# Kernel optimization log

Hardware: AMD Instinct MI355X
Metric: run time of the kernel (lower is better)

Reference implementation:

```python
import jax, jax.numpy as jnp
import numpy as np


def _apply_rope(t, cos, sin):
    # t: [b, s, h, d]; cos/sin: [s, d//2]; interleaved complex rotation
    b, s, h, d = t.shape
    tr = t.reshape(b, s, h, d // 2, 2)
    a, bb = tr[..., 0], tr[..., 1]
    c = cos[None, :, None, :]
    si = sin[None, :, None, :]
    out_r = a * c - bb * si
    out_i = a * si + bb * c
    return jnp.stack([out_r, out_i], axis=-1).reshape(b, s, h, d)


def setup_inputs() -> dict:
    key = jax.random.key(0)
    ks = jax.random.split(key, 10)
    B, S, D = 4, 512, 4096
    H, HKV, HD = 32, 8, 128
    START = 512
    wscale = 0.02  # keep activations in sane range
    x = jax.random.normal(ks[0], (B, S, D), dtype=jnp.float32)
    wq = jax.random.normal(ks[1], (H * HD, D), dtype=jnp.float32) * wscale
    wk = jax.random.normal(ks[2], (HKV * HD, D), dtype=jnp.float32) * wscale
    wv = jax.random.normal(ks[3], (HKV * HD, D), dtype=jnp.float32) * wscale
    wo = jax.random.normal(ks[4], (D, H * HD), dtype=jnp.float32) * wscale
    # RoPE angles for absolute positions [START, START+S)
    theta = 500000.0
    inv_freq = 1.0 / (theta ** (np.arange(0, HD, 2, dtype=np.float32) / HD))
    pos = np.arange(START, START + S, dtype=np.float32)
    ang = pos[:, None] * inv_freq[None, :]  # [S, HD//2]
    freqs_cos = jnp.asarray(np.cos(ang), dtype=jnp.float32)
    freqs_sin = jnp.asarray(np.sin(ang), dtype=jnp.float32)
    cache_k = jax.random.normal(ks[5], (B, START, HKV, HD), dtype=jnp.float32)
    cache_v = jax.random.normal(ks[6], (B, START, HKV, HD), dtype=jnp.float32)
    return {"x": x, "wq": wq, "wk": wk, "wv": wv, "wo": wo,
            "freqs_cos": freqs_cos, "freqs_sin": freqs_sin,
            "cache_k": cache_k, "cache_v": cache_v, "start_pos": START}


def reference(x, wq, wk, wv, wo, freqs_cos, freqs_sin, cache_k, cache_v, start_pos):
    B, S, D = x.shape
    H = wq.shape[0] // 128
    HKV = wk.shape[0] // 128
    HD = 128
    n_rep = H // HKV
    # QKV projections (Linear: y = x @ W^T)
    xq = jnp.einsum('bsd,ed->bse', x, wq).reshape(B, S, H, HD)
    xk = jnp.einsum('bsd,ed->bse', x, wk).reshape(B, S, HKV, HD)
    xv = jnp.einsum('bsd,ed->bse', x, wv).reshape(B, S, HKV, HD)
    # rotary embedding on new q/k
    xq = _apply_rope(xq, freqs_cos, freqs_sin)
    xk = _apply_rope(xk, freqs_cos, freqs_sin)
    # append new k/v to cache -> total kv length T = start_pos + S
    keys = jnp.concatenate([cache_k, xk], axis=1)    # [B, T, HKV, HD]
    values = jnp.concatenate([cache_v, xv], axis=1)  # [B, T, HKV, HD]
    # GQA: repeat kv heads (repeat_interleave along head dim)
    keys = jnp.repeat(keys, n_rep, axis=2)      # [B, T, H, HD]
    values = jnp.repeat(values, n_rep, axis=2)  # [B, T, H, HD]
    scores = jnp.einsum('bqhd,bkhd->bhqk', xq, keys) / jnp.sqrt(jnp.float32(HD))
    # causal mask: query abs pos start_pos+i attends to kv pos <= start_pos+i
    T = start_pos + S
    q_pos = start_pos + jnp.arange(S)
    k_pos = jnp.arange(T)
    mask = k_pos[None, :] <= q_pos[:, None]  # [S, T]
    scores = jnp.where(mask[None, None, :, :], scores, -jnp.inf)
    probs = jax.nn.softmax(scores.astype(jnp.float32), axis=-1).astype(x.dtype)
    out = jnp.einsum('bhqk,bkhd->bqhd', probs, values).reshape(B, S, H * HD)
    return jnp.einsum('bse,de->bsd', out, wo)
```

## Files before the change

### kernel.cpp

```cpp
#include <hip/hip_runtime.h>
#include <hip/hip_bf16.h>


#define B_ 4
#define S_ 512
#define D_ 4096
#define H_ 32
#define HKV_ 8
#define HD_ 128
#define T_ 1024
#define M_ 2048
#define NQKV_ 6144

typedef __attribute__((ext_vector_type(8))) short bf16x8;
typedef __attribute__((ext_vector_type(4))) float f32x4;

#define GLOAD_LDS16(g, l)                                                     \
  __builtin_amdgcn_global_load_lds(                                           \
      (const __attribute__((address_space(1))) void*)(g),                     \
      (__attribute__((address_space(3))) void*)(l), 16, 0, 0)

__device__ __forceinline__ void st_c(float* p, float v) { *p = v; }
__device__ __forceinline__ void st_c(__hip_bfloat16* p, float v) {
  *p = __float2bfloat16(v);
}

__global__ void cvt_f32_bf16(const float* __restrict__ in,
                             __hip_bfloat16* __restrict__ out, long n) {
  long i = ((long)blockIdx.x * blockDim.x + threadIdx.x) * 4;
  if (i >= n) return;
  float4 v = *(const float4*)(in + i);
  __hip_bfloat16 t[4] = {__float2bfloat16(v.x), __float2bfloat16(v.y),
                         __float2bfloat16(v.z), __float2bfloat16(v.w)};
  *(uint2*)(out + i) = *(const uint2*)t;
}

template <typename CT>
__global__ __launch_bounds__(256) void gemm_nt(
    const __hip_bfloat16* __restrict__ A, const __hip_bfloat16* __restrict__ B,
    CT* __restrict__ C, int M, int N, int K, long ldA, long ldB, long ldC,
    int Hdiv, int rep, long sAb, long sAh, long sBb, long sBh, long sCb,
    long sCh) {
  int z = blockIdx.z;
  int zb = z / Hdiv, zh = z - zb * Hdiv;
  A += (long)zb * sAb + (long)zh * sAh;
  B += (long)zb * sBb + (long)(zh / rep) * sBh;
  C += (long)zb * sCb + (long)zh * sCh;

  const int m0 = blockIdx.y * 128;
  const int n0 = blockIdx.x * 128;
  const int tid = threadIdx.x;
  const int wave = tid >> 6, lane = tid & 63;
  const int wm = (wave >> 1) * 64, wn = (wave & 1) * 64;

  __shared__ __align__(16) __hip_bfloat16 As[128 * 32];
  __shared__ __align__(16) __hip_bfloat16 Bs[128 * 32];

  const int slot0 = tid, slot1 = 256 + tid;
  const int r0 = slot0 >> 2, c0 = (slot0 & 3) ^ ((r0 >> 1) & 3);
  const int r1 = slot1 >> 2, c1 = (slot1 & 3) ^ ((r1 >> 1) & 3);
  const __hip_bfloat16* gA0 = A + (long)(m0 + r0) * ldA + c0 * 8;
  const __hip_bfloat16* gA1 = A + (long)(m0 + r1) * ldA + c1 * 8;
  const __hip_bfloat16* gB0 = B + (long)(n0 + r0) * ldB + c0 * 8;
  const __hip_bfloat16* gB1 = B + (long)(n0 + r1) * ldB + c1 * 8;
  __hip_bfloat16* sA0 = &As[wave * 512];
  __hip_bfloat16* sA1 = &As[2048 + wave * 512];
  __hip_bfloat16* sB0 = &Bs[wave * 512];
  __hip_bfloat16* sB1 = &Bs[2048 + wave * 512];

  const int lr = lane & 15;
  const int sfrag = (lane >> 4) ^ ((lr >> 1) & 3);
  const int abase = (wm + lr) * 32 + sfrag * 8;
  const int bbase = (wn + lr) * 32 + sfrag * 8;

  f32x4 acc[4][4];
#pragma unroll
  for (int i = 0; i < 4; i++)
#pragma unroll
    for (int j = 0; j < 4; j++) acc[i][j] = f32x4{0.f, 0.f, 0.f, 0.f};

  for (int kt = 0; kt < K; kt += 32) {
    GLOAD_LDS16(gA0, sA0);
    GLOAD_LDS16(gA1, sA1);
    GLOAD_LDS16(gB0, sB0);
    GLOAD_LDS16(gB1, sB1);
    gA0 += 32;
    gA1 += 32;
    gB0 += 32;
    gB1 += 32;
    __syncthreads();

    bf16x8 af[4], bfv[4];
#pragma unroll
    for (int i = 0; i < 4; i++) {
      af[i] = *(const bf16x8*)&As[abase + i * 512];
      bfv[i] = *(const bf16x8*)&Bs[bbase + i * 512];
    }
#pragma unroll
    for (int i = 0; i < 4; i++)
#pragma unroll
      for (int j = 0; j < 4; j++)
        acc[i][j] =
            __builtin_amdgcn_mfma_f32_16x16x32_bf16(af[i], bfv[j], acc[i][j],
                                                    0, 0, 0);
    __syncthreads();
  }

  const int crow0 = m0 + wm + (lane >> 4) * 4;
  const int ccol0 = n0 + wn + (lane & 15);
#pragma unroll
  for (int i = 0; i < 4; i++)
#pragma unroll
    for (int j = 0; j < 4; j++)
#pragma unroll
      for (int r = 0; r < 4; r++)
        st_c(&C[(long)(crow0 + i * 16 + r) * ldC + (ccol0 + j * 16)],
             acc[i][j][r]);
}

__global__ __launch_bounds__(256, 2) void flash_attn(
    const __hip_bfloat16* __restrict__ qb,
    const __hip_bfloat16* __restrict__ kb,
    const __hip_bfloat16* __restrict__ vtb,
    __hip_bfloat16* __restrict__ ob) {
  const int qt = 3 - blockIdx.x;
  const int z = blockIdx.y;
  const int b = z >> 5, h = z & 31, kvh = h >> 2;
  const int q0 = qt * 128;
  const int tid = threadIdx.x, wave = tid >> 6, lane = tid & 63;
  const int lr = lane & 15, lq = lane >> 4;
  const int wrow = wave * 32;
  const float scale = 0.08838834764831845f;

  __shared__ __align__(16) __hip_bfloat16 smem[64 * 128 + 128 * 64 + 128 * 72];
  __hip_bfloat16* Ks = smem;
  __hip_bfloat16* Vs = smem + 64 * 128;
  __hip_bfloat16* Ps = smem + 64 * 128 + 128 * 64;
  __hip_bfloat16* Os = smem;

  const __hip_bfloat16* Kz = kb + ((long)(b * 8 + kvh)) * T_ * HD_;
  const __hip_bfloat16* Vz = vtb + ((long)(b * 8 + kvh)) * HD_ * T_;
  const __hip_bfloat16* Qz = qb + ((long)(b * 512 + q0)) * 4096 + h * 128;
  __hip_bfloat16* obz = ob + ((long)(b * 512 + q0)) * 4096 + h * 128;

  bf16x8 qf[2][4];
#pragma unroll
  for (int i = 0; i < 2; i++)
#pragma unroll
    for (int kb4 = 0; kb4 < 4; kb4++)
      qf[i][kb4] = *(const bf16x8*)(Qz + (long)(wrow + i * 16 + lr) * 4096 +
                                    kb4 * 32 + lq * 8);

  int kOff[4], vOff[4];
#pragma unroll
  for (int it = 0; it < 4; it++) {
    int G = it * 256 + tid;
    int t = G >> 4, ck = (G & 15) ^ (t & 7);
    kOff[it] = t * 128 + ck * 8;
    int d = G >> 3, cv = (G & 7) ^ (d & 7);
    vOff[it] = d * 1024 + cv * 8;
  }

  f32x4 O[2][8];
#pragma unroll
  for (int i = 0; i < 2; i++)
#pragma unroll
    for (int j = 0; j < 8; j++) O[i][j] = f32x4{0.f, 0.f, 0.f, 0.f};
  float mst[2][4], lst[2][4];
#pragma unroll
  for (int i = 0; i < 2; i++)
#pragma unroll
    for (int r = 0; r < 4; r++) {
      mst[i][r] = -1e30f;
      lst[i][r] = 0.f;
    }

  const int ntiles = 10 + 2 * qt, fulltiles = 8 + 2 * qt;
  const int hxor = lr & 7;

  for (int kt = 0; kt < ntiles; kt++) {
    const int k0 = kt * 64;
#pragma unroll
    for (int it = 0; it < 4; it++)
      GLOAD_LDS16(Kz + (long)k0 * 128 + kOff[it],
                  Ks + (it * 256 + wave * 64) * 8);
#pragma unroll
    for (int it = 0; it < 4; it++)
      GLOAD_LDS16(Vz + k0 + vOff[it], Vs + (it * 256 + wave * 64) * 8);
    __syncthreads();

    f32x4 s[2][4];
#pragma unroll
    for (int i = 0; i < 2; i++)
#pragma unroll
      for (int j = 0; j < 4; j++) s[i][j] = f32x4{0.f, 0.f, 0.f, 0.f};
#pragma unroll
    for (int kb4 = 0; kb4 < 4; kb4++) {
      bf16x8 kf[4];
#pragma unroll
      for (int j = 0; j < 4; j++)
        kf[j] = *(const bf16x8*)(Ks + (j * 16 + lr) * 128 +
                                 ((kb4 * 4 + lq) ^ hxor) * 8);
#pragma unroll
      for (int i = 0; i < 2; i++)
#pragma unroll
        for (int j = 0; j < 4; j++)
          s[i][j] = __builtin_amdgcn_mfma_f32_16x16x32_bf16(qf[i][kb4], kf[j],
                                                            s[i][j], 0, 0, 0);
    }

    const bool mt = (kt >= fulltiles);
#pragma unroll
    for (int i = 0; i < 2; i++)
#pragma unroll
      for (int j = 0; j < 4; j++)
#pragma unroll
        for (int r = 0; r < 4; r++) {
          float sv = s[i][j][r] * scale;
          if (mt) {
            int key = k0 + j * 16 + lr;
            int qp = 512 + q0 + wrow + i * 16 + lq * 4 + r;
            if (key > qp) sv = -1e30f;
          }
          s[i][j][r] = sv;
        }

    float al[2][4];
#pragma unroll
    for (int i = 0; i < 2; i++)
#pragma unroll
      for (int r = 0; r < 4; r++) {
        float mx = fmaxf(fmaxf(s[i][0][r], s[i][1][r]),
                         fmaxf(s[i][2][r], s[i][3][r]));
        mx = fmaxf(mx, __shfl_xor(mx, 1));
        mx = fmaxf(mx, __shfl_xor(mx, 2));
        mx = fmaxf(mx, __shfl_xor(mx, 4));
        mx = fmaxf(mx, __shfl_xor(mx, 8));
        float mn = fmaxf(mst[i][r], mx);
        al[i][r] = __expf(mst[i][r] - mn);
        mst[i][r] = mn;
      }
#pragma unroll
    for (int i = 0; i < 2; i++)
#pragma unroll
      for (int j = 0; j < 4; j++)
#pragma unroll
        for (int r = 0; r < 4; r++)
          s[i][j][r] = __expf(s[i][j][r] - mst[i][r]);
#pragma unroll
    for (int i = 0; i < 2; i++)
#pragma unroll
      for (int r = 0; r < 4; r++) {
        float sm = s[i][0][r] + s[i][1][r] + s[i][2][r] + s[i][3][r];
        sm += __shfl_xor(sm, 1);
        sm += __shfl_xor(sm, 2);
        sm += __shfl_xor(sm, 4);
        sm += __shfl_xor(sm, 8);
        lst[i][r] = lst[i][r] * al[i][r] + sm;
      }
#pragma unroll
    for (int i = 0; i < 2; i++)
#pragma unroll
      for (int j = 0; j < 8; j++)
#pragma unroll
        for (int r = 0; r < 4; r++) O[i][j][r] *= al[i][r];

#pragma unroll
    for (int i = 0; i < 2; i++)
#pragma unroll
      for (int j = 0; j < 4; j++)
#pragma unroll
        for (int r = 0; r < 4; r++)
          Ps[(wrow + i * 16 + lq * 4 + r) * 72 + j * 16 + lr] =
              __float2bfloat16(s[i][j][r]);

#pragma unroll
    for (int kc = 0; kc < 2; kc++) {
      bf16x8 pa[2];
#pragma unroll
      for (int i = 0; i < 2; i++)
        pa[i] = *(const bf16x8*)(Ps + (wrow + i * 16 + lr) * 72 + kc * 32 +
                                 lq * 8);
      bf16x8 vf[8];
#pragma unroll
      for (int j = 0; j < 8; j++)
        vf[j] = *(const bf16x8*)(Vs + (j * 16 + lr) * 64 +
                                 ((kc * 4 + lq) ^ hxor) * 8);
#pragma unroll
      for (int i = 0; i < 2; i++)
#pragma unroll
        for (int j = 0; j < 8; j++)
          O[i][j] = __builtin_amdgcn_mfma_f32_16x16x32_bf16(pa[i], vf[j],
                                                            O[i][j], 0, 0, 0);
    }
    __syncthreads();
  }

#pragma unroll
  for (int i = 0; i < 2; i++)
#pragma unroll
    for (int r = 0; r < 4; r++) {
      float inv = 1.f / lst[i][r];
#pragma unroll
      for (int j = 0; j < 8; j++)
        Os[(wrow + i * 16 + lq * 4 + r) * 136 + j * 16 + lr] =
            __float2bfloat16(O[i][j][r] * inv);
    }
  __syncthreads();
#pragma unroll
  for (int it = 0; it < 8; it++) {
    int G = it * 256 + tid;
    int m = G >> 4, c = G & 15;
    *(bf16x8*)(obz + (long)m * 4096 + c * 8) =
        *(const bf16x8*)(Os + m * 136 + c * 8);
  }
}

__global__ void rope_kernel(const float* __restrict__ qkv,
                            const float* __restrict__ fcos,
                            const float* __restrict__ fsin,
                            __hip_bfloat16* __restrict__ qb,
                            __hip_bfloat16* __restrict__ kb) {
  int m = blockIdx.y;
  int j = blockIdx.x * blockDim.x + threadIdx.x;
  if (j >= 2560) return;
  int s = m & (S_ - 1);
  long rowbase = (long)m * NQKV_;
  if (j < 2048) {
    int dpair = j & 63;
    float a = qkv[rowbase + 2 * j], bb = qkv[rowbase + 2 * j + 1];
    float c = fcos[s * 64 + dpair], si = fsin[s * 64 + dpair];
    long o = (long)m * 4096 + 2 * j;
    qb[o] = __float2bfloat16(a * c - bb * si);
    qb[o + 1] = __float2bfloat16(a * si + bb * c);
  } else {
    int j2 = j - 2048;
    int kvh = j2 >> 6, dpair = j2 & 63;
    float a = qkv[rowbase + 4096 + 2 * j2], bb = qkv[rowbase + 4096 + 2 * j2 + 1];
    float c = fcos[s * 64 + dpair], si = fsin[s * 64 + dpair];
    int b = m >> 9;
    long o = (((long)(b * HKV_ + kvh)) * T_ + 512 + s) * HD_ + 2 * dpair;
    kb[o] = __float2bfloat16(a * c - bb * si);
    kb[o + 1] = __float2bfloat16(a * si + bb * c);
  }
}

__global__ void kcache_cvt(const float* __restrict__ cache_k,
                           __hip_bfloat16* __restrict__ kb) {
  long i = (long)blockIdx.x * 256 + threadIdx.x;
  if (i >= (long)B_ * HKV_ * 512 * HD_) return;
  int d = i & 127;
  int t = (i >> 7) & 511;
  int kvh = (i >> 16) & 7;
  int b = i >> 19;
  long o = (((long)(b * HKV_ + kvh)) * T_ + t) * HD_ + d;
  kb[o] = __float2bfloat16(
      cache_k[(((long)(b * 512 + t)) * HKV_ + kvh) * HD_ + d]);
}

__global__ void v_transpose(const float* __restrict__ cache_v,
                            const float* __restrict__ qkv,
                            __hip_bfloat16* __restrict__ vtb) {
  __shared__ float tile[32][33];
  int t0 = blockIdx.x * 32, d0 = blockIdx.y * 32;
  int bk = blockIdx.z;
  int b = bk >> 3, kvh = bk & 7;
#pragma unroll
  for (int it = 0; it < 4; it++) {
    int t = t0 + threadIdx.y + it * 8;
    int d = d0 + threadIdx.x;
    float v;
    if (t < 512)
      v = cache_v[(((long)(b * 512 + t)) * HKV_ + kvh) * HD_ + d];
    else
      v = qkv[((long)(b * S_) + (t - 512)) * NQKV_ + 5120 + kvh * HD_ + d];
    tile[threadIdx.y + it * 8][threadIdx.x] = v;
  }
  __syncthreads();
#pragma unroll
  for (int it = 0; it < 4; it++) {
    int d = d0 + threadIdx.y + it * 8;
    int t = t0 + threadIdx.x;
    vtb[((long)bk * HD_ + d) * T_ + t] =
        __float2bfloat16(tile[threadIdx.x][threadIdx.y + it * 8]);
  }
}

extern "C" void kernel_launch(void* const* d_in, const int* in_sizes, int n_in,
                              void* d_out, int out_size, void* d_ws,
                              size_t ws_size, hipStream_t stream) {
  const float* x = (const float*)d_in[0];
  const float* wq = (const float*)d_in[1];
  const float* wk = (const float*)d_in[2];
  const float* wv = (const float*)d_in[3];
  const float* wo = (const float*)d_in[4];
  const float* fcos = (const float*)d_in[5];
  const float* fsin = (const float*)d_in[6];
  const float* cache_k = (const float*)d_in[7];
  const float* cache_v = (const float*)d_in[8];
  float* out = (float*)d_out;

  char* ws = (char*)d_ws;
  const size_t szR0 = (size_t)M_ * 4096 * 2;
  const size_t szR1 = (size_t)NQKV_ * D_ * 2;
  const size_t szR2 = (size_t)M_ * NQKV_ * 4;
  const size_t szKV = (size_t)B_ * HKV_ * T_ * HD_ * 2;

  size_t R0 = 0;
  size_t R1 = R0 + szR0;
  size_t R2 = R1 + szR1;
  size_t R3 = R2 + szR2;
  size_t R4 = R3 + szKV;

  __hip_bfloat16* xb = (__hip_bfloat16*)(ws + R0);
  __hip_bfloat16* wqkvb = (__hip_bfloat16*)(ws + R1);
  float* qkvf = (float*)(ws + R2);
  __hip_bfloat16* kb = (__hip_bfloat16*)(ws + R3);
  __hip_bfloat16* vtb = (__hip_bfloat16*)(ws + R4);

  dim3 blk(256);

  cvt_f32_bf16<<<(M_ * (long)D_ / 4 + 255) / 256, blk, 0, stream>>>(
      x, xb, (long)M_ * D_);
  cvt_f32_bf16<<<((long)D_ * D_ / 4 + 255) / 256, blk, 0, stream>>>(
      wq, wqkvb, (long)D_ * D_);
  cvt_f32_bf16<<<((long)1024 * D_ / 4 + 255) / 256, blk, 0, stream>>>(
      wk, wqkvb + (long)4096 * D_, (long)1024 * D_);
  cvt_f32_bf16<<<((long)1024 * D_ / 4 + 255) / 256, blk, 0, stream>>>(
      wv, wqkvb + (long)5120 * D_, (long)1024 * D_);

  gemm_nt<float><<<dim3(NQKV_ / 128, M_ / 128, 1), blk, 0, stream>>>(
      xb, wqkvb, qkvf, M_, NQKV_, D_, D_, D_, NQKV_, 1, 1, 0, 0, 0, 0, 0, 0);

  __hip_bfloat16* qb = xb;
  rope_kernel<<<dim3(10, M_), blk, 0, stream>>>(qkvf, fcos, fsin, qb, kb);

  kcache_cvt<<<((long)B_ * HKV_ * 512 * HD_ + 255) / 256, blk, 0, stream>>>(
      cache_k, kb);
  v_transpose<<<dim3(T_ / 32, HD_ / 32, B_ * HKV_), dim3(32, 8), 0, stream>>>(
      cache_v, qkvf, vtb);

  __hip_bfloat16* wob = wqkvb;
  cvt_f32_bf16<<<((long)D_ * D_ / 4 + 255) / 256, blk, 0, stream>>>(
      wo, wob, (long)D_ * D_);

  __hip_bfloat16* ob = xb;
  flash_attn<<<dim3(4, B_ * H_), blk, 0, stream>>>(qb, kb, vtb, ob);

  gemm_nt<float><<<dim3(D_ / 128, M_ / 128, 1), blk, 0, stream>>>(
      ob, wob, out, M_, D_, D_, D_, D_, D_, 1, 1, 0, 0, 0, 0, 0, 0);
}
```

Baseline: 560.6 us.

## Replace 128x128 GEMM with double-buffered 256x256 tile GEMM with XCD swizzle

The QKV and output projections now use a new GEMM with 256x256 tiles, 512 threads and a 64-wide K step. The K step is split into two 32-wide halves across a double-buffered LDS ring, so global-to-LDS loads for the next tile are issued while MFMAs on the current tile run. Barriers and s_setprio raise the priority of the MFMA phases. The workgroup index is remapped so neighbouring tiles land on the same XCD for L2 reuse. The aim is to cut the load/compute serialisation and global traffic of the old single-buffered kernel, at the cost of more LDS (128KB) and more registers per block.

```diff
diff --git a/kernel.cpp b/kernel.cpp
--- a/kernel.cpp
+++ b/kernel.cpp
@@ -20,11 +20,6 @@
       (const __attribute__((address_space(1))) void*)(g),                     \
       (__attribute__((address_space(3))) void*)(l), 16, 0, 0)
 
-__device__ __forceinline__ void st_c(float* p, float v) { *p = v; }
-__device__ __forceinline__ void st_c(__hip_bfloat16* p, float v) {
-  *p = __float2bfloat16(v);
-}
-
 __global__ void cvt_f32_bf16(const float* __restrict__ in,
                              __hip_bfloat16* __restrict__ out, long n) {
   long i = ((long)blockIdx.x * blockDim.x + threadIdx.x) * 4;
@@ -35,87 +30,154 @@
   *(uint2*)(out + i) = *(const uint2*)t;
 }
 
-template <typename CT>
-__global__ __launch_bounds__(256) void gemm_nt(
+__global__ __launch_bounds__(512, 2) void gemm256(
     const __hip_bfloat16* __restrict__ A, const __hip_bfloat16* __restrict__ B,
-    CT* __restrict__ C, int M, int N, int K, long ldA, long ldB, long ldC,
-    int Hdiv, int rep, long sAb, long sAh, long sBb, long sBh, long sCb,
-    long sCh) {
-  int z = blockIdx.z;
-  int zb = z / Hdiv, zh = z - zb * Hdiv;
-  A += (long)zb * sAb + (long)zh * sAh;
-  B += (long)zb * sBb + (long)(zh / rep) * sBh;
-  C += (long)zb * sCb + (long)zh * sCh;
-
-  const int m0 = blockIdx.y * 128;
-  const int n0 = blockIdx.x * 128;
+    float* __restrict__ C, int M, int N, int K, long ldA, long ldB, long ldC) {
+  const int nbx = N >> 8;
+  const int nwg = nbx * (M >> 8);
+  const int lin = blockIdx.x + nbx * blockIdx.y;
+  const int cpx = nwg >> 3;
+  const int swz = (lin & 7) * cpx + (lin >> 3);
+  const int m0 = (swz / nbx) << 8;
+  const int n0 = (swz - (swz / nbx) * nbx) << 8;
+
   const int tid = threadIdx.x;
-  const int wave = tid >> 6, lane = tid & 63;
-  const int wm = (wave >> 1) * 64, wn = (wave & 1) * 64;
-
-  __shared__ __align__(16) __hip_bfloat16 As[128 * 32];
-  __shared__ __align__(16) __hip_bfloat16 Bs[128 * 32];
-
-  const int slot0 = tid, slot1 = 256 + tid;
-  const int r0 = slot0 >> 2, c0 = (slot0 & 3) ^ ((r0 >> 1) & 3);
-  const int r1 = slot1 >> 2, c1 = (slot1 & 3) ^ ((r1 >> 1) & 3);
-  const __hip_bfloat16* gA0 = A + (long)(m0 + r0) * ldA + c0 * 8;
-  const __hip_bfloat16* gA1 = A + (long)(m0 + r1) * ldA + c1 * 8;
-  const __hip_bfloat16* gB0 = B + (long)(n0 + r0) * ldB + c0 * 8;
-  const __hip_bfloat16* gB1 = B + (long)(n0 + r1) * ldB + c1 * 8;
-  __hip_bfloat16* sA0 = &As[wave * 512];
-  __hip_bfloat16* sA1 = &As[2048 + wave * 512];
-  __hip_bfloat16* sB0 = &Bs[wave * 512];
-  __hip_bfloat16* sB1 = &Bs[2048 + wave * 512];
-
-  const int lr = lane & 15;
-  const int sfrag = (lane >> 4) ^ ((lr >> 1) & 3);
-  const int abase = (wm + lr) * 32 + sfrag * 8;
-  const int bbase = (wn + lr) * 32 + sfrag * 8;
-
-  f32x4 acc[4][4];
-#pragma unroll
-  for (int i = 0; i < 4; i++)
+  const int w = tid >> 6, l = tid & 63;
+  const int wm = w >> 2, wn = w & 3;
+  const int lr = l & 15, lq = l >> 4;
+
+  __shared__ __align__(16) __hip_bfloat16 smem[8][8192];
+
+  const int rS = w * 16 + (l >> 2);
+  const int cS = (l & 3) ^ ((rS >> 1) & 3);
+  const __hip_bfloat16* gA = A + (long)(m0 + rS) * ldA + cS * 8;
+  const __hip_bfloat16* gB = B + (long)(n0 + rS) * ldB + cS * 8;
+  const long stA = 128 * ldA, stB = 128 * ldB;
+  const int wofs = w * 512;
+
+  const int cR = (lq ^ ((lr >> 1) & 3)) * 8;
+  const int aOff = (wm * 128 + lr) * 32 + cR;
+  const int bOff = (wn * 64 + lr) * 32 + cR;
+
+  f32x4 acc[8][4];
+#pragma unroll
+  for (int i = 0; i < 8; i++)
 #pragma unroll
     for (int j = 0; j < 4; j++) acc[i][j] = f32x4{0.f, 0.f, 0.f, 0.f};
 
-  for (int kt = 0; kt < K; kt += 32) {
-    GLOAD_LDS16(gA0, sA0);
-    GLOAD_LDS16(gA1, sA1);
-    GLOAD_LDS16(gB0, sB0);
-    GLOAD_LDS16(gB1, sB1);
-    gA0 += 32;
-    gA1 += 32;
-    gB0 += 32;
-    gB1 += 32;
-    __syncthreads();
-
-    bf16x8 af[4], bfv[4];
-#pragma unroll
-    for (int i = 0; i < 4; i++) {
-      af[i] = *(const bf16x8*)&As[abase + i * 512];
-      bfv[i] = *(const bf16x8*)&Bs[bbase + i * 512];
-    }
+  const int nkt = K >> 6;
+
+#define STAGE_A(buf, kh, ko)                                  \
+  {                                                           \
+    const __hip_bfloat16* g_ = gA + (ko) + (kh) * 32;         \
+    __hip_bfloat16* d_ = &smem[(buf) * 4 + (kh)][wofs];       \
+    GLOAD_LDS16(g_, d_);                                      \
+    GLOAD_LDS16(g_ + stA, d_ + 4096);                         \
+  }
+#define STAGE_B(buf, kh, ko)                                  \
+  {                                                           \
+    const __hip_bfloat16* g_ = gB + (ko) + (kh) * 32;         \
+    __hip_bfloat16* d_ = &smem[(buf) * 4 + 2 + (kh)][wofs];   \
+    GLOAD_LDS16(g_, d_);                                      \
+    GLOAD_LDS16(g_ + stB, d_ + 4096);                         \
+  }
+
+  STAGE_A(0, 0, 0);
+  STAGE_B(0, 0, 0);
+  STAGE_A(0, 1, 0);
+  STAGE_B(0, 1, 0);
+  asm volatile("s_waitcnt vmcnt(4)" ::: "memory");
+  __builtin_amdgcn_s_barrier();
+
+  bf16x8 af[4], bfr[4];
+  for (int t = 0; t < nkt; ++t) {
+    const int b = t & 1;
+    int tn = t + 1;
+    if (tn == nkt) tn = 0;
+    const long ko = (long)tn << 6;
+    const __hip_bfloat16* rA0 = &smem[b * 4 + 0][0];
+    const __hip_bfloat16* rA1 = &smem[b * 4 + 1][0];
+    const __hip_bfloat16* rB0 = &smem[b * 4 + 2][0];
+    const __hip_bfloat16* rB1 = &smem[b * 4 + 3][0];
+
+#pragma unroll
+    for (int i = 0; i < 4; i++) af[i] = *(const bf16x8*)(rA0 + aOff + i * 512);
+#pragma unroll
+    for (int j = 0; j < 4; j++) bfr[j] = *(const bf16x8*)(rB0 + bOff + j * 512);
+    STAGE_A(b ^ 1, 0, ko);
+    __builtin_amdgcn_s_barrier();
+    __builtin_amdgcn_s_setprio(1);
 #pragma unroll
     for (int i = 0; i < 4; i++)
 #pragma unroll
       for (int j = 0; j < 4; j++)
-        acc[i][j] =
-            __builtin_amdgcn_mfma_f32_16x16x32_bf16(af[i], bfv[j], acc[i][j],
-                                                    0, 0, 0);
-    __syncthreads();
-  }
-
-  const int crow0 = m0 + wm + (lane >> 4) * 4;
-  const int ccol0 = n0 + wn + (lane & 15);
-#pragma unroll
-  for (int i = 0; i < 4; i++)
+        acc[i][j] = __builtin_amdgcn_mfma_f32_16x16x32_bf16(af[i], bfr[j],
+                                                            acc[i][j], 0, 0, 0);
+    __builtin_amdgcn_s_setprio(0);
+    __builtin_amdgcn_s_barrier();
+
+#pragma unroll
+    for (int i = 0; i < 4; i++)
+      af[i] = *(const bf16x8*)(rA0 + aOff + (i + 4) * 512);
+    STAGE_B(b ^ 1, 0, ko);
+    asm volatile("s_waitcnt vmcnt(4)" ::: "memory");
+    __builtin_amdgcn_s_barrier();
+    __builtin_amdgcn_s_setprio(1);
+#pragma unroll
+    for (int i = 0; i < 4; i++)
+#pragma unroll
+      for (int j = 0; j < 4; j++)
+        acc[i + 4][j] = __builtin_amdgcn_mfma_f32_16x16x32_bf16(
+            af[i], bfr[j], acc[i + 4][j], 0, 0, 0);
+    __builtin_amdgcn_s_setprio(0);
+    __builtin_amdgcn_s_barrier();
+
+#pragma unroll
+    for (int i = 0; i < 4; i++) af[i] = *(const bf16x8*)(rA1 + aOff + i * 512);
+#pragma unroll
+    for (int j = 0; j < 4; j++) bfr[j] = *(const bf16x8*)(rB1 + bOff + j * 512);
+    STAGE_A(b ^ 1, 1, ko);
+    __builtin_amdgcn_s_barrier();
+    __builtin_amdgcn_s_setprio(1);
+#pragma unroll
+    for (int i = 0; i < 4; i++)
+#pragma unroll
+      for (int j = 0; j < 4; j++)
+        acc[i][j] = __builtin_amdgcn_mfma_f32_16x16x32_bf16(af[i], bfr[j],
+                                                            acc[i][j], 0, 0, 0);
+    __builtin_amdgcn_s_setprio(0);
+    __builtin_amdgcn_s_barrier();
+
+#pragma unroll
+    for (int i = 0; i < 4; i++)
+      af[i] = *(const bf16x8*)(rA1 + aOff + (i + 4) * 512);
+    STAGE_B(b ^ 1, 1, ko);
+    asm volatile("s_waitcnt vmcnt(4)" ::: "memory");
+    __builtin_amdgcn_s_barrier();
+    __builtin_amdgcn_s_setprio(1);
+#pragma unroll
+    for (int i = 0; i < 4; i++)
+#pragma unroll
+      for (int j = 0; j < 4; j++)
+        acc[i + 4][j] = __builtin_amdgcn_mfma_f32_16x16x32_bf16(
+            af[i], bfr[j], acc[i + 4][j], 0, 0, 0);
+    __builtin_amdgcn_s_setprio(0);
+    __builtin_amdgcn_s_barrier();
+  }
+  asm volatile("s_waitcnt vmcnt(0)" ::: "memory");
+
+#undef STAGE_A
+#undef STAGE_B
+
+  const int crow = m0 + wm * 128 + lq * 4;
+  const int ccol = n0 + wn * 64 + lr;
+#pragma unroll
+  for (int i = 0; i < 8; i++)
 #pragma unroll
     for (int j = 0; j < 4; j++)
 #pragma unroll
       for (int r = 0; r < 4; r++)
-        st_c(&C[(long)(crow0 + i * 16 + r) * ldC + (ccol0 + j * 16)],
-             acc[i][j][r]);
+        C[(long)(crow + i * 16 + r) * ldC + (ccol + j * 16)] = acc[i][j][r];
 }
 
 __global__ __launch_bounds__(256, 2) void flash_attn(
@@ -429,8 +491,8 @@
   cvt_f32_bf16<<<((long)1024 * D_ / 4 + 255) / 256, blk, 0, stream>>>(
       wv, wqkvb + (long)5120 * D_, (long)1024 * D_);
 
-  gemm_nt<float><<<dim3(NQKV_ / 128, M_ / 128, 1), blk, 0, stream>>>(
-      xb, wqkvb, qkvf, M_, NQKV_, D_, D_, D_, NQKV_, 1, 1, 0, 0, 0, 0, 0, 0);
+  gemm256<<<dim3(NQKV_ / 256, M_ / 256), dim3(512), 0, stream>>>(
+      xb, wqkvb, qkvf, M_, NQKV_, D_, D_, D_, NQKV_);
 
   __hip_bfloat16* qb = xb;
   rope_kernel<<<dim3(10, M_), blk, 0, stream>>>(qkvf, fcos, fsin, qb, kb);
@@ -447,6 +509,6 @@
   __hip_bfloat16* ob = xb;
   flash_attn<<<dim3(4, B_ * H_), blk, 0, stream>>>(qb, kb, vtb, ob);
 
-  gemm_nt<float><<<dim3(D_ / 128, M_ / 128, 1), blk, 0, stream>>>(
-      ob, wob, out, M_, D_, D_, D_, D_, D_, 1, 1, 0, 0, 0, 0, 0, 0);
-}
+  gemm256<<<dim3(D_ / 256, M_ / 256), dim3(512), 0, stream>>>(
+      ob, wob, out, M_, D_, D_, D_, D_, D_);
+}
```

After: 526.9 us. -6.0%, faster.
